# Optimization experiments

Hardware: AMD Instinct MI355X
Metric: run time of the kernel (lower is better)

## Reference

```python
import jax, jax.numpy as jnp
import numpy as np

N_NODES = 100000
N_EDGES = 1600000
FEAT_DIM = 64
IN_DIM = FEAT_DIM + 3  # feat + xyz


def setup_inputs() -> dict:
    key = jax.random.key(0)
    k1, k2, k3, k4, k5 = jax.random.split(key, 5)
    xyz = jax.random.normal(k1, (N_NODES, 3), dtype=jnp.float32)
    feat = jax.random.normal(k2, (N_NODES, FEAT_DIM), dtype=jnp.float32)
    edge_index = jax.random.randint(k3, (2, N_EDGES), 0, N_NODES, dtype=jnp.int64)
    # MLP params (Linear stored as [in, out] for x @ W + b)
    W1 = jax.random.normal(k4, (2 * IN_DIM, FEAT_DIM), dtype=jnp.float32) * (1.0 / np.sqrt(2 * IN_DIM))
    b1 = jnp.zeros((FEAT_DIM,), dtype=jnp.float32)
    W2 = jax.random.normal(k5, (FEAT_DIM, FEAT_DIM), dtype=jnp.float32) * (1.0 / np.sqrt(FEAT_DIM))
    b2 = jnp.zeros((FEAT_DIM,), dtype=jnp.float32)
    return {"xyz": xyz, "feat": feat, "edge_index": edge_index,
            "W1": W1, "b1": b1, "W2": W2, "b2": b2}


def reference(xyz, feat, edge_index, W1, b1, W2, b2):
    # node features: cat([feat, xyz]) -> [N, C+3]
    x = jnp.concatenate([feat, xyz], axis=-1)
    src = edge_index[0]  # j (source / neighbor)
    dst = edge_index[1]  # i (target, aggregation index)
    x_i = x[dst]                       # [E, C+3]
    x_j = x[src]                       # [E, C+3]
    # EdgeConv message: mlp(cat([x_i, x_j - x_i]))
    m = jnp.concatenate([x_i, x_j - x_i], axis=-1)   # [E, 2*(C+3)]
    h = jax.nn.relu(m @ W1 + b1) @ W2 + b2           # [E, C]
    n = x.shape[0]
    agg = jax.ops.segment_max(h, dst, num_segments=n)  # [N, C]
    # nodes with no incoming edges get 0 (matches PyG scatter-max fill)
    deg = jax.ops.segment_sum(jnp.ones((dst.shape[0],), h.dtype), dst, num_segments=n)
    return jnp.where(deg[:, None] > 0, agg, jnp.zeros_like(agg))
```

## Files before the change

### kernel.cpp

```cpp
#include <hip/hip_runtime.h>
#include <stdint.h>

#define N_NODES 100000
#define FEAT 64
#define NB 64
#define SC_CHUNK 8192
#define NBKT 1563
#define BKT_CAP 1400
#define RVN 6
#define BIAS 512.0f
#define NT_NODES 128
#define XT_STRIDE 132
#define SMEM_BYTES (67 * XT_STRIDE * 4 + 2 * 67 * 64 * 4)

typedef __attribute__((ext_vector_type(8))) _Float16 half8;
typedef __attribute__((ext_vector_type(2))) _Float16 half2v;
typedef __attribute__((ext_vector_type(2))) __fp16 fp16x2;
typedef __attribute__((ext_vector_type(4))) float f32x4;

__device__ __forceinline__ uint32_t enc_key(float f) {
    uint32_t u = __float_as_uint(f);
    return (u & 0x80000000u) ? ~u : (u | 0x80000000u);
}
__device__ __forceinline__ float dec_key(uint32_t k) {
    return __uint_as_float((k & 0x80000000u) ? (k & 0x7FFFFFFFu) : ~k);
}
__device__ __forceinline__ uint32_t pk_f16(float a, float b) {
    union { fp16x2 h; uint32_t u; } cv;
    cv.h = __builtin_amdgcn_cvt_pkrtz(a, b);
    return cv.u;
}

#define W2T_OFF 0
#define AMB_OFF 4096
#define BM_OFF  8384
#define W2P_OFF 12672
#define U_OFF   16384
#define V_OFF   (U_OFF + N_NODES * FEAT / 2)
#define GCNT_OFF (U_OFF + N_NODES * FEAT)
#define SRT_OFF  (GCNT_OFF + 2048)

__global__ __launch_bounds__(256) void transform_kernel(
    const float* __restrict__ W1, const float* __restrict__ W2,
    float* __restrict__ ws, int full)
{
    int i = blockIdx.x * 256 + threadIdx.x;
    if (full && i < 2048)
        ((uint32_t*)ws)[GCNT_OFF + i] = 0u;
    if (i < 4096) {
        int c2 = i >> 6, c = i & 63;
        ws[W2T_OFF + i] = W2[c * 64 + c2];
    } else if (full && i < 8384) {
        int j = i - 4096;
        ws[AMB_OFF + j] = W1[j] - W1[j + 67 * 64];
    } else if (full && i < 12672) {
        int j = i - 8384;
        ws[BM_OFF + j] = W1[j + 67 * 64];
    } else if (full && i < 16768) {
        int p = i - 12672;
        int j = p & 7, c2lo = (p >> 3) & 15, quad = (p >> 7) & 3;
        int h = (p >> 9) & 1, n4 = (p >> 10) & 3;
        int k = h * 32 + quad * 8 + j;
        int n = n4 * 16 + c2lo;
        ((_Float16*)(ws + W2P_OFF))[p] = (_Float16)W2[k * 64 + n];
    }
}

__global__ __launch_bounds__(256) void nodebkt_kernel(
    const float* __restrict__ xyz, const float* __restrict__ feat,
    const float* __restrict__ b1, const float* __restrict__ ws,
    uint16_t* __restrict__ U, uint16_t* __restrict__ V, int nN,
    const int* __restrict__ ei, uint32_t* __restrict__ gcnt,
    uint32_t* __restrict__ sorted, int nE, int nBkt)
{
    extern __shared__ float smem[];
    int t = threadIdx.x;

    if ((int)blockIdx.x < nBkt) {
        uint32_t* hist = (uint32_t*)smem;
        int e0 = blockIdx.x * SC_CHUNK;
        int cnt = min(SC_CHUNK, nE - e0);
        int cnt4 = cnt & ~3;

        for (int i = t; i < NBKT; i += 256) hist[i] = 0;
        __syncthreads();
        for (int i = t * 4; i < cnt4; i += 1024) {
            uint4 d4 = *(const uint4*)(ei + nE + e0 + i);
            atomicAdd(&hist[d4.x >> 6], 1u);
            atomicAdd(&hist[d4.y >> 6], 1u);
            atomicAdd(&hist[d4.z >> 6], 1u);
            atomicAdd(&hist[d4.w >> 6], 1u);
        }
        for (int i = cnt4 + t; i < cnt; i += 256)
            atomicAdd(&hist[ei[nE + e0 + i] >> 6], 1u);
        __syncthreads();
        for (int b = t; b < NBKT; b += 256) {
            uint32_t c = hist[b];
            hist[b] = c ? atomicAdd(&gcnt[b], c) : 0u;
        }
        __syncthreads();
        for (int i = t * 4; i < cnt4; i += 1024) {
            uint4 s4 = *(const uint4*)(ei + e0 + i);
            uint4 d4 = *(const uint4*)(ei + nE + e0 + i);
            uint32_t sa[4] = {(uint32_t)s4.x, (uint32_t)s4.y, (uint32_t)s4.z, (uint32_t)s4.w};
            uint32_t da[4] = {(uint32_t)d4.x, (uint32_t)d4.y, (uint32_t)d4.z, (uint32_t)d4.w};
            #pragma unroll
            for (int k = 0; k < 4; ++k) {
                uint32_t b = da[k] >> 6;
                uint32_t pos = atomicAdd(&hist[b], 1u);
                if (pos < BKT_CAP)
                    sorted[(size_t)b * BKT_CAP + pos] = sa[k] | ((da[k] & 63u) << 20);
            }
        }
        for (int i = cnt4 + t; i < cnt; i += 256) {
            uint32_t src = (uint32_t)ei[e0 + i];
            uint32_t dst = (uint32_t)ei[nE + e0 + i];
            uint32_t b = dst >> 6;
            uint32_t pos = atomicAdd(&hist[b], 1u);
            if (pos < BKT_CAP)
                sorted[(size_t)b * BKT_CAP + pos] = src | ((dst & 63u) << 20);
        }
        return;
    }

    float* xt = smem;
    float* wA = smem + 67 * XT_STRIDE;
    float* wB = wA + 67 * 64;

    int nb0 = ((int)blockIdx.x - nBkt) * NT_NODES;
    int rows = min(NT_NODES, nN - nb0);

    for (int i4 = t; i4 < 67 * 16; i4 += 256) {
        *(float4*)(wA + i4 * 4) = *(const float4*)(ws + AMB_OFF + i4 * 4);
        *(float4*)(wB + i4 * 4) = *(const float4*)(ws + BM_OFF + i4 * 4);
    }
    for (int g4 = t; g4 < rows * 16; g4 += 256) {
        int row = g4 >> 4, c4 = (g4 & 15) * 4;
        float4 v = *(const float4*)(feat + (size_t)(nb0 + row) * FEAT + c4);
        xt[(c4 + 0) * XT_STRIDE + row] = v.x;
        xt[(c4 + 1) * XT_STRIDE + row] = v.y;
        xt[(c4 + 2) * XT_STRIDE + row] = v.z;
        xt[(c4 + 3) * XT_STRIDE + row] = v.w;
    }
    for (int i = t; i < 3 * NT_NODES; i += 256) {
        int k3 = i >> 7, row = i & 127;
        float v = (row < rows) ? xyz[(size_t)(nb0 + row) * 3 + k3] : 0.0f;
        xt[(64 + k3) * XT_STRIDE + row] = v;
    }
    __syncthreads();

    int cb = (t & 15) * 4;
    int ng = (t >> 4) * 8;

    float accU[8][4], accV[8][4];
    #pragma unroll
    for (int c = 0; c < 4; ++c) {
        float bv = b1[cb + c];
        #pragma unroll
        for (int r = 0; r < 8; ++r) { accU[r][c] = bv; accV[r][c] = 0.0f; }
    }

    const float* xrow = xt + ng;
    #pragma unroll 2
    for (int k = 0; k < 67; ++k) {
        float4 x0 = *(const float4*)(xrow + k * XT_STRIDE);
        float4 x1 = *(const float4*)(xrow + k * XT_STRIDE + 4);
        float4 wa = *(const float4*)(wA + k * 64 + cb);
        float4 wb = *(const float4*)(wB + k * 64 + cb);
        float xv[8] = {x0.x, x0.y, x0.z, x0.w, x1.x, x1.y, x1.z, x1.w};
        float wav[4] = {wa.x, wa.y, wa.z, wa.w};
        float wbv[4] = {wb.x, wb.y, wb.z, wb.w};
        #pragma unroll
        for (int r = 0; r < 8; ++r) {
            #pragma unroll
            for (int c = 0; c < 4; ++c) {
                accU[r][c] = fmaf(xv[r], wav[c], accU[r][c]);
                accV[r][c] = fmaf(xv[r], wbv[c], accV[r][c]);
            }
        }
    }

    #pragma unroll
    for (int r = 0; r < 8; ++r) {
        if (ng + r < rows) {
            size_t n = (size_t)(nb0 + ng + r);
            uint2 oU; oU.x = pk_f16(accU[r][0], accU[r][1]);
                      oU.y = pk_f16(accU[r][2], accU[r][3]);
            *(uint2*)(U + n * FEAT + cb) = oU;
            uint2 oV; oV.x = pk_f16(accV[r][0], accV[r][1]);
                      oV.y = pk_f16(accV[r][2], accV[r][3]);
            *(uint2*)(V + n * FEAT + cb) = oV;
        }
    }
}

#define LOADE(G, DSV, VV0, VV1, UU0, UU1) do {                               \
        int e_c_ = min((G) + el, cnt - 1);                                   \
        uint32_t val_ = ssrt[e_c_];                                          \
        DSV = *(const uint4*)(ssrt + (G) + quad * 4);                        \
        int src_ = (int)(val_ & 0xFFFFFu);                                   \
        const uint32_t* vr_ = (const uint32_t*)(V + (size_t)src_ * FEAT);    \
        VV0 = *(const uint4*)(vr_ + quad * 4);                               \
        VV1 = *(const uint4*)(vr_ + 16 + quad * 4);                          \
        const uint32_t* ur_ = ushare + (int)(val_ >> 20) * 32;               \
        UU0 = *(const uint4*)(ur_ + quad * 4);                               \
        UU1 = *(const uint4*)(ur_ + 16 + quad * 4);                          \
    } while (0)

__global__ __launch_bounds__(256) void agg_kernel(
    const uint32_t* __restrict__ gcnt, const uint32_t* __restrict__ sorted,
    const uint16_t* __restrict__ U, const uint16_t* __restrict__ V,
    const float* __restrict__ ws_w2p, const float* __restrict__ b2,
    float* __restrict__ out, int nN)
{
    __shared__ int      lmax[NB * 65];
    __shared__ uint32_t ushare[NB * 32];
    __shared__ uint32_t ssrt[BKT_CAP + 16];
    __shared__ uint32_t shist[NB];

    int bkt = blockIdx.x;
    int nb0 = bkt * NB;
    int rows = min(NB, nN - nb0);
    int cnt = min((int)gcnt[bkt], BKT_CAP);
    int t = threadIdx.x;

    for (int i = t; i < NB * 65; i += 256) lmax[i] = 0;
    if (t < NB) shist[t] = 0;
    {
        const uint4* usrc4 = (const uint4*)(U + (size_t)nb0 * FEAT);
        for (int i = t; i < rows * 8; i += 256) ((uint4*)ushare)[i] = usrc4[i];
    }
    const uint32_t* bsrc = sorted + (size_t)bkt * BKT_CAP;
    __syncthreads();

    uint32_t rv[RVN];
    #pragma unroll
    for (int j = 0; j < RVN; ++j) {
        int i = t + j * 256;
        if (i < cnt) {
            uint32_t v = bsrc[i];
            rv[j] = v;
            atomicAdd(&shist[v >> 20], 1u);
        }
    }
    __syncthreads();
    if (t < NB) {
        uint32_t v = shist[t];
        uint32_t run = v;
        #pragma unroll
        for (int d = 1; d < 64; d <<= 1) {
            uint32_t x = (uint32_t)__shfl_up((int)run, (unsigned)d, 64);
            if (t >= d) run += x;
        }
        shist[t] = run - v;
    }
    __syncthreads();
    #pragma unroll
    for (int j = 0; j < RVN; ++j) {
        int i = t + j * 256;
        if (i < cnt) {
            uint32_t v = rv[j];
            uint32_t pos = atomicAdd(&shist[v >> 20], 1u);
            ssrt[pos] = v;
        }
    }
    __syncthreads();

    int lane = t & 63;
    int wave = t >> 6;
    int el = lane & 15, quad = lane >> 4;

    const uint4* w2p = (const uint4*)ws_w2p;
    union { uint4 u4; half8 h8; } bfr[8];
    #pragma unroll
    for (int q8 = 0; q8 < 8; ++q8)
        bfr[q8].u4 = w2p[(q8 * 4 + quad) * 16 + el];
    float b2v[4];
    #pragma unroll
    for (int n4 = 0; n4 < 4; ++n4) b2v[n4] = b2[n4 * 16 + el] + BIAS;

    const half2v zero2 = {(_Float16)0.0f, (_Float16)0.0f};

    uint4 dsv_c, vv_c0, vv_c1, uu_c0, uu_c1;
    int g = wave * 16;
    if (g < cnt) LOADE(g, dsv_c, vv_c0, vv_c1, uu_c0, uu_c1);

    #pragma unroll 1
    for (; g < cnt; g += 64) {
        int gn = g + 64;
        int gl = (gn < cnt) ? gn : g;
        uint4 dsv_n, vv_n0, vv_n1, uu_n0, uu_n1;
        LOADE(gl, dsv_n, vv_n0, vv_n1, uu_n0, uu_n1);

        union { uint4 u4; half8 h8; } afr[2];
        #pragma unroll
        for (int h = 0; h < 2; ++h) {
            uint4 uu = h ? uu_c1 : uu_c0;
            uint4 vv = h ? vv_c1 : vv_c0;
            uint32_t ua[4] = {uu.x, uu.y, uu.z, uu.w};
            uint32_t va[4] = {vv.x, vv.y, vv.z, vv.w};
            uint32_t pk[4];
            #pragma unroll
            for (int p = 0; p < 4; ++p) {
                union { uint32_t u; half2v h2; } cu, cv2, ct;
                cu.u = ua[p]; cv2.u = va[p];
                ct.h2 = __builtin_elementwise_max(cu.h2 + cv2.h2, zero2);
                pk[p] = ct.u;
            }
            afr[h].u4 = make_uint4(pk[0], pk[1], pk[2], pk[3]);
        }

        f32x4 acc[4];
        #pragma unroll
        for (int n4 = 0; n4 < 4; ++n4)
            acc[n4] = (f32x4){b2v[n4], b2v[n4], b2v[n4], b2v[n4]};
        #pragma unroll
        for (int n4 = 0; n4 < 4; ++n4) {
            acc[n4] = __builtin_amdgcn_mfma_f32_16x16x32_f16(afr[0].h8, bfr[n4*2+0].h8, acc[n4], 0, 0, 0);
            acc[n4] = __builtin_amdgcn_mfma_f32_16x16x32_f16(afr[1].h8, bfr[n4*2+1].h8, acc[n4], 0, 0, 0);
        }

        int d0 = (int)(dsv_c.x >> 20), d1 = (int)(dsv_c.y >> 20);
        int d2 = (int)(dsv_c.z >> 20), d3 = (int)(dsv_c.w >> 20);
        int eb = g + quad * 4;
        bool ok0 = eb < cnt, ok1 = eb + 1 < cnt;
        bool ok2 = eb + 2 < cnt, ok3 = eb + 3 < cnt;
        bool m0 = (d0 == d1) & ok1;
        bool m1 = (d1 == d2) & ok2;
        bool m2 = (d2 == d3) & ok3;
        #pragma unroll
        for (int n4 = 0; n4 < 4; ++n4) {
            if (m0) acc[n4][1] = fmaxf(acc[n4][1], acc[n4][0]);
            if (m1) acc[n4][2] = fmaxf(acc[n4][2], acc[n4][1]);
            if (m2) acc[n4][3] = fmaxf(acc[n4][3], acc[n4][2]);
        }
        if (ok0 & !m0) {
            #pragma unroll
            for (int n4 = 0; n4 < 4; ++n4)
                atomicMax(&lmax[d0 * 65 + n4 * 16 + el], __float_as_int(acc[n4][0]));
        }
        if (ok1 & !m1) {
            #pragma unroll
            for (int n4 = 0; n4 < 4; ++n4)
                atomicMax(&lmax[d1 * 65 + n4 * 16 + el], __float_as_int(acc[n4][1]));
        }
        if (ok2 & !m2) {
            #pragma unroll
            for (int n4 = 0; n4 < 4; ++n4)
                atomicMax(&lmax[d2 * 65 + n4 * 16 + el], __float_as_int(acc[n4][2]));
        }
        if (ok3) {
            #pragma unroll
            for (int n4 = 0; n4 < 4; ++n4)
                atomicMax(&lmax[d3 * 65 + n4 * 16 + el], __float_as_int(acc[n4][3]));
        }

        dsv_c = dsv_n;
        vv_c0 = vv_n0; vv_c1 = vv_n1;
        uu_c0 = uu_n0; uu_c1 = uu_n1;
    }
    __syncthreads();

    for (int i = t * 4; i < rows * FEAT; i += 1024) {
        int r = i >> 6, c = i & 63;
        int lb = r * 65 + c;
        int k0 = lmax[lb + 0], k1 = lmax[lb + 1];
        int k2 = lmax[lb + 2], k3 = lmax[lb + 3];
        float4 o;
        o.x = k0 ? (__int_as_float(k0) - BIAS) : 0.0f;
        o.y = k1 ? (__int_as_float(k1) - BIAS) : 0.0f;
        o.z = k2 ? (__int_as_float(k2) - BIAS) : 0.0f;
        o.w = k3 ? (__int_as_float(k3) - BIAS) : 0.0f;
        *(float4*)(out + (size_t)(nb0 + r) * FEAT + c) = o;
    }
}
#undef LOADE

__device__ __forceinline__ void rank1_update(
    float* __restrict__ h, float xi, float d,
    const float* __restrict__ A, const float* __restrict__ B)
{
    #pragma unroll
    for (int c = 0; c < FEAT; ++c)
        h[c] = fmaf(xi, A[c], fmaf(d, B[c], h[c]));
}

__global__ __launch_bounds__(256) void edge_fused_kernel(
    const float* __restrict__ xyz, const float* __restrict__ feat,
    const int* __restrict__ ei,
    const float* __restrict__ W1, const float* __restrict__ b1,
    const float* __restrict__ ws, const float* __restrict__ b2,
    uint32_t* __restrict__ keys, int nE)
{
    int e = blockIdx.x * 256 + threadIdx.x;
    if (e >= nE) return;
    int src = ei[e];
    int dst = ei[nE + e];
    const float* __restrict__ W2T = ws + W2T_OFF;

    float h[FEAT];
    #pragma unroll
    for (int c = 0; c < FEAT; ++c) h[c] = b1[c];

    const float* fi = feat + (size_t)dst * FEAT;
    const float* fj = feat + (size_t)src * FEAT;
    #pragma unroll 1
    for (int k = 0; k < 64; k += 4) {
        float4 a = *(const float4*)(fi + k);
        float4 b = *(const float4*)(fj + k);
        rank1_update(h, a.x, b.x - a.x, W1 + (k + 0) * 64, W1 + (67 + k + 0) * 64);
        rank1_update(h, a.y, b.y - a.y, W1 + (k + 1) * 64, W1 + (67 + k + 1) * 64);
        rank1_update(h, a.z, b.z - a.z, W1 + (k + 2) * 64, W1 + (67 + k + 2) * 64);
        rank1_update(h, a.w, b.w - a.w, W1 + (k + 3) * 64, W1 + (67 + k + 3) * 64);
    }
    {
        const float* pi = xyz + (size_t)dst * 3;
        const float* pj = xyz + (size_t)src * 3;
        #pragma unroll
        for (int k3 = 0; k3 < 3; ++k3) {
            float xi = pi[k3];
            rank1_update(h, xi, pj[k3] - xi, W1 + (64 + k3) * 64, W1 + (131 + k3) * 64);
        }
    }
    #pragma unroll
    for (int c = 0; c < FEAT; ++c) h[c] = fmaxf(h[c], 0.0f);

    uint32_t* krow = keys + (size_t)dst * FEAT;
    #pragma unroll 1
    for (int c2 = 0; c2 < FEAT; c2 += 4) {
        float o0 = b2[c2 + 0], o1 = b2[c2 + 1];
        float o2 = b2[c2 + 2], o3 = b2[c2 + 3];
        const float* w0 = W2T + (c2 + 0) * 64;
        const float* w1 = W2T + (c2 + 1) * 64;
        const float* w2 = W2T + (c2 + 2) * 64;
        const float* w3 = W2T + (c2 + 3) * 64;
        #pragma unroll
        for (int c = 0; c < FEAT; ++c) {
            float hv = h[c];
            o0 = fmaf(hv, w0[c], o0);
            o1 = fmaf(hv, w1[c], o1);
            o2 = fmaf(hv, w2[c], o2);
            o3 = fmaf(hv, w3[c], o3);
        }
        uint32_t k0 = enc_key(o0), k1 = enc_key(o1);
        uint32_t k2 = enc_key(o2), k3 = enc_key(o3);
        uint4 cur = *(const uint4*)(krow + c2);
        if (k0 > cur.x) atomicMax(&krow[c2 + 0], k0);
        if (k1 > cur.y) atomicMax(&krow[c2 + 1], k1);
        if (k2 > cur.z) atomicMax(&krow[c2 + 2], k2);
        if (k3 > cur.w) atomicMax(&krow[c2 + 3], k3);
    }
}

__global__ __launch_bounds__(256) void decode_kernel(
    uint32_t* __restrict__ keys, int n4)
{
    int i = blockIdx.x * 256 + threadIdx.x;
    if (i >= n4) return;
    uint4 k = ((const uint4*)keys)[i];
    float4 r;
    r.x = k.x ? dec_key(k.x) : 0.0f;
    r.y = k.y ? dec_key(k.y) : 0.0f;
    r.z = k.z ? dec_key(k.z) : 0.0f;
    r.w = k.w ? dec_key(k.w) : 0.0f;
    ((float4*)keys)[i] = r;
}

extern "C" void kernel_launch(void* const* d_in, const int* in_sizes, int n_in,
                              void* d_out, int out_size, void* d_ws, size_t ws_size,
                              hipStream_t stream)
{
    const float* xyz  = (const float*)d_in[0];
    const float* feat = (const float*)d_in[1];
    const int*   ei   = (const int*)d_in[2];
    const float* W1   = (const float*)d_in[3];
    const float* b1   = (const float*)d_in[4];
    const float* W2   = (const float*)d_in[5];
    const float* b2   = (const float*)d_in[6];

    int nE = in_sizes[2] / 2;
    float* ws = (float*)d_ws;

    size_t need_words = (size_t)SRT_OFF + (size_t)NBKT * BKT_CAP;
    int full = (ws_size >= need_words * 4) ? 1 : 0;

    transform_kernel<<<66, 256, 0, stream>>>(W1, W2, ws, full);

    if (full) {
        uint16_t* U = (uint16_t*)(ws + U_OFF);
        uint16_t* V = (uint16_t*)(ws + V_OFF);
        uint32_t* gcnt   = (uint32_t*)(ws + GCNT_OFF);
        uint32_t* sorted = (uint32_t*)(ws + SRT_OFF);

        int nBkt = (nE + SC_CHUNK - 1) / SC_CHUNK;
        int nodeBlocks = (N_NODES + NT_NODES - 1) / NT_NODES;
        nodebkt_kernel<<<nBkt + nodeBlocks, 256, SMEM_BYTES, stream>>>(
            xyz, feat, b1, ws, U, V, N_NODES, ei, gcnt, sorted, nE, nBkt);
        agg_kernel<<<NBKT, 256, 0, stream>>>(
            gcnt, sorted, U, V, ws + W2P_OFF, b2, (float*)d_out, N_NODES);
    } else {
        uint32_t* keys = (uint32_t*)d_out;
        hipMemsetAsync(d_out, 0, (size_t)out_size * sizeof(float), stream);
        edge_fused_kernel<<<(nE + 255) / 256, 256, 0, stream>>>(
            xyz, feat, ei, W1, b1, ws, b2, keys, nE);
        decode_kernel<<<(out_size / 4 + 255) / 256, 256, 0, stream>>>(
            keys, out_size / 4);
    }
}
```

Baseline: 174.1 us.

## Fold weight preprocessing into node/bucket kernel and halve node tile size

```diff
diff --git a/kernel.cpp b/kernel.cpp
--- a/kernel.cpp
+++ b/kernel.cpp
@@ -9,8 +9,8 @@
 #define BKT_CAP 1400
 #define RVN 6
 #define BIAS 512.0f
-#define NT_NODES 128
-#define XT_STRIDE 132
+#define NT_NODES 64
+#define XT_STRIDE 68
 #define SMEM_BYTES (67 * XT_STRIDE * 4 + 2 * 67 * 64 * 4)
 
 typedef __attribute__((ext_vector_type(8))) _Float16 half8;
@@ -45,33 +45,19 @@
     float* __restrict__ ws, int full)
 {
     int i = blockIdx.x * 256 + threadIdx.x;
-    if (full && i < 2048)
-        ((uint32_t*)ws)[GCNT_OFF + i] = 0u;
     if (i < 4096) {
         int c2 = i >> 6, c = i & 63;
         ws[W2T_OFF + i] = W2[c * 64 + c2];
-    } else if (full && i < 8384) {
-        int j = i - 4096;
-        ws[AMB_OFF + j] = W1[j] - W1[j + 67 * 64];
-    } else if (full && i < 12672) {
-        int j = i - 8384;
-        ws[BM_OFF + j] = W1[j + 67 * 64];
-    } else if (full && i < 16768) {
-        int p = i - 12672;
-        int j = p & 7, c2lo = (p >> 3) & 15, quad = (p >> 7) & 3;
-        int h = (p >> 9) & 1, n4 = (p >> 10) & 3;
-        int k = h * 32 + quad * 8 + j;
-        int n = n4 * 16 + c2lo;
-        ((_Float16*)(ws + W2P_OFF))[p] = (_Float16)W2[k * 64 + n];
     }
 }
 
 __global__ __launch_bounds__(256) void nodebkt_kernel(
     const float* __restrict__ xyz, const float* __restrict__ feat,
-    const float* __restrict__ b1, const float* __restrict__ ws,
+    const float* __restrict__ b1, const float* __restrict__ W1,
+    const float* __restrict__ W2, float* __restrict__ ws,
     uint16_t* __restrict__ U, uint16_t* __restrict__ V, int nN,
     const int* __restrict__ ei, uint32_t* __restrict__ gcnt,
-    uint32_t* __restrict__ sorted, int nE, int nBkt)
+    uint32_t* __restrict__ sorted, int nE, int nBkt, int nodeBlocks)
 {
     extern __shared__ float smem[];
     int t = threadIdx.x;
@@ -123,16 +109,33 @@
         return;
     }
 
+    int nb = (int)blockIdx.x - nBkt;
+    if (nb >= nodeBlocks) {
+        int p = (nb - nodeBlocks) * 256 + t;
+        if (p < 4096) {
+            int j = p & 7, c2lo = (p >> 3) & 15, quad = (p >> 7) & 3;
+            int h = (p >> 9) & 1, n4 = (p >> 10) & 3;
+            int k = h * 32 + quad * 8 + j;
+            int n = n4 * 16 + c2lo;
+            ((_Float16*)(ws + W2P_OFF))[p] = (_Float16)W2[k * 64 + n];
+        }
+        return;
+    }
+
     float* xt = smem;
     float* wA = smem + 67 * XT_STRIDE;
     float* wB = wA + 67 * 64;
 
-    int nb0 = ((int)blockIdx.x - nBkt) * NT_NODES;
+    int nb0 = nb * NT_NODES;
     int rows = min(NT_NODES, nN - nb0);
 
     for (int i4 = t; i4 < 67 * 16; i4 += 256) {
-        *(float4*)(wA + i4 * 4) = *(const float4*)(ws + AMB_OFF + i4 * 4);
-        *(float4*)(wB + i4 * 4) = *(const float4*)(ws + BM_OFF + i4 * 4);
+        float4 a = *(const float4*)(W1 + i4 * 4);
+        float4 b = *(const float4*)(W1 + 67 * 64 + i4 * 4);
+        float4 d;
+        d.x = a.x - b.x; d.y = a.y - b.y; d.z = a.z - b.z; d.w = a.w - b.w;
+        *(float4*)(wA + i4 * 4) = d;
+        *(float4*)(wB + i4 * 4) = b;
     }
     for (int g4 = t; g4 < rows * 16; g4 += 256) {
         int row = g4 >> 4, c4 = (g4 & 15) * 4;
@@ -143,35 +146,34 @@
         xt[(c4 + 3) * XT_STRIDE + row] = v.w;
     }
     for (int i = t; i < 3 * NT_NODES; i += 256) {
-        int k3 = i >> 7, row = i & 127;
+        int k3 = i >> 6, row = i & 63;
         float v = (row < rows) ? xyz[(size_t)(nb0 + row) * 3 + k3] : 0.0f;
         xt[(64 + k3) * XT_STRIDE + row] = v;
     }
     __syncthreads();
 
     int cb = (t & 15) * 4;
-    int ng = (t >> 4) * 8;
-
-    float accU[8][4], accV[8][4];
+    int ng = (t >> 4) * 4;
+
+    float accU[4][4], accV[4][4];
     #pragma unroll
     for (int c = 0; c < 4; ++c) {
         float bv = b1[cb + c];
         #pragma unroll
-        for (int r = 0; r < 8; ++r) { accU[r][c] = bv; accV[r][c] = 0.0f; }
+        for (int r = 0; r < 4; ++r) { accU[r][c] = bv; accV[r][c] = 0.0f; }
     }
 
     const float* xrow = xt + ng;
     #pragma unroll 2
     for (int k = 0; k < 67; ++k) {
         float4 x0 = *(const float4*)(xrow + k * XT_STRIDE);
-        float4 x1 = *(const float4*)(xrow + k * XT_STRIDE + 4);
         float4 wa = *(const float4*)(wA + k * 64 + cb);
         float4 wb = *(const float4*)(wB + k * 64 + cb);
-        float xv[8] = {x0.x, x0.y, x0.z, x0.w, x1.x, x1.y, x1.z, x1.w};
+        float xv[4] = {x0.x, x0.y, x0.z, x0.w};
         float wav[4] = {wa.x, wa.y, wa.z, wa.w};
         float wbv[4] = {wb.x, wb.y, wb.z, wb.w};
         #pragma unroll
-        for (int r = 0; r < 8; ++r) {
+        for (int r = 0; r < 4; ++r) {
             #pragma unroll
             for (int c = 0; c < 4; ++c) {
                 accU[r][c] = fmaf(xv[r], wav[c], accU[r][c]);
@@ -181,7 +183,7 @@
     }
 
     #pragma unroll
-    for (int r = 0; r < 8; ++r) {
+    for (int r = 0; r < 4; ++r) {
         if (ng + r < rows) {
             size_t n = (size_t)(nb0 + ng + r);
             uint2 oU; oU.x = pk_f16(accU[r][0], accU[r][1]);
@@ -484,22 +486,24 @@
     size_t need_words = (size_t)SRT_OFF + (size_t)NBKT * BKT_CAP;
     int full = (ws_size >= need_words * 4) ? 1 : 0;
 
-    transform_kernel<<<66, 256, 0, stream>>>(W1, W2, ws, full);
-
     if (full) {
         uint16_t* U = (uint16_t*)(ws + U_OFF);
         uint16_t* V = (uint16_t*)(ws + V_OFF);
         uint32_t* gcnt   = (uint32_t*)(ws + GCNT_OFF);
         uint32_t* sorted = (uint32_t*)(ws + SRT_OFF);
 
+        hipMemsetAsync(gcnt, 0, NBKT * sizeof(uint32_t), stream);
         int nBkt = (nE + SC_CHUNK - 1) / SC_CHUNK;
         int nodeBlocks = (N_NODES + NT_NODES - 1) / NT_NODES;
-        nodebkt_kernel<<<nBkt + nodeBlocks, 256, SMEM_BYTES, stream>>>(
-            xyz, feat, b1, ws, U, V, N_NODES, ei, gcnt, sorted, nE, nBkt);
+        int packBlocks = 16;
+        nodebkt_kernel<<<nBkt + nodeBlocks + packBlocks, 256, SMEM_BYTES, stream>>>(
+            xyz, feat, b1, W1, W2, ws, U, V, N_NODES, ei, gcnt, sorted, nE,
+            nBkt, nodeBlocks);
         agg_kernel<<<NBKT, 256, 0, stream>>>(
             gcnt, sorted, U, V, ws + W2P_OFF, b2, (float*)d_out, N_NODES);
     } else {
         uint32_t* keys = (uint32_t*)d_out;
+        transform_kernel<<<16, 256, 0, stream>>>(W1, W2, ws, 0);
         hipMemsetAsync(d_out, 0, (size_t)out_size * sizeof(float), stream);
         edge_fused_kernel<<<(nE + 255) / 256, 256, 0, stream>>>(
             xyz, feat, ei, W1, b1, ws, b2, keys, nE);
```

Measured after the change: 173.5 us. About the same (-0.4%).
